# Kernel tuning notes

Measured on AMD Instinct MI355X. Metric: run time of the kernel, lower is better.

## Reference

```python
import jax, jax.numpy as jnp
import numpy as np

FEAT = 2048
NUM_CLASSES = 751
EPS = 1e-5


def setup_inputs() -> dict:
    key = jax.random.key(0)
    k1, k2, k3 = jax.random.split(key, 3)
    probe_x = jax.random.normal(k1, (64, FEAT), dtype=jnp.float32)
    gallery_x = jax.random.normal(k2, (256, FEAT), dtype=jnp.float32)
    # BatchNorm1d affine params (PyTorch init: gamma=1, beta=0)
    bn_gamma = jnp.ones((FEAT,), dtype=jnp.float32)
    bn_beta = jnp.zeros((FEAT,), dtype=jnp.float32)
    # classifier: weight ~ N(0, 0.001), bias = 0
    W = jax.random.normal(k3, (NUM_CLASSES, FEAT), dtype=jnp.float32) * 0.001
    b = jnp.zeros((NUM_CLASSES,), dtype=jnp.float32)
    return {"probe_x": probe_x, "gallery_x": gallery_x,
            "bn_gamma": bn_gamma, "bn_beta": bn_beta, "W": W, "b": b}


def reference(probe_x, gallery_x, bn_gamma, bn_beta, W, b):
    n_probe, feat = probe_x.shape
    n_gallery = gallery_x.shape[0]
    # broadcast squared difference: [Np, Ng, F]
    diff = jnp.square(probe_x[:, None, :] - gallery_x[None, :, :])
    d = diff.reshape(n_probe * n_gallery, feat)
    # BatchNorm1d in training mode: biased batch statistics over the batch dim
    mean = jnp.mean(d, axis=0)
    var = jnp.mean(jnp.square(d - mean), axis=0)
    bn = (d - mean) * (bn_gamma / jnp.sqrt(var + EPS)) + bn_beta
    # Linear classifier
    cls = jnp.einsum('nf,cf->nc', bn, W) + b
    return cls.reshape(n_probe, n_gallery, -1)
```

## Files before the change

kernel.cpp:

```cpp
#include <hip/hip_runtime.h>
#include <hip/hip_bf16.h>
#include <hip/hip_fp16.h>

#define FEAT 2048
#define NCLS 751
#define NPAD 768
#define NPRB 64
#define NGAL 256
#define WSCALE 256.0f

typedef _Float16 f16x8 __attribute__((ext_vector_type(8)));
typedef float f32x4 __attribute__((ext_vector_type(4)));

__device__ __forceinline__ unsigned short f2h_u(float x) {
  union { _Float16 h; unsigned short u; } v;
  v.h = (_Float16)x;
  return v.u;
}

__global__ __launch_bounds__(256)
void stats_kernel(const float* __restrict__ P, const float* __restrict__ G,
                  const float* __restrict__ gamma, const float* __restrict__ beta,
                  float* __restrict__ st) {
  const int t = threadIdx.x;
  const int fx = t & 7, ry = t >> 3;
  const int f = blockIdx.x * 8 + fx;
  float a1 = 0, a2 = 0, a3 = 0, a4 = 0;
#pragma unroll
  for (int r = ry; r < NPRB; r += 32) {
    float x = P[r * FEAT + f], x2 = x * x;
    a1 += x; a2 += x2; a3 += x2 * x; a4 += x2 * x2;
  }
  float b1 = 0, b2 = 0, b3 = 0, b4 = 0;
#pragma unroll
  for (int r = ry; r < NGAL; r += 32) {
    float x = G[r * FEAT + f], x2 = x * x;
    b1 += x; b2 += x2; b3 += x2 * x; b4 += x2 * x2;
  }
  __shared__ float red[8][32][8];
  __shared__ float red2[8][4][8];
  float vals[8] = {a1, a2, a3, a4, b1, b2, b3, b4};
#pragma unroll
  for (int m = 0; m < 8; ++m) red[m][ry][fx] = vals[m];
  __syncthreads();
  {
    int m = t >> 5, q = (t >> 3) & 3, fx2 = t & 7;
    float s = 0.f;
#pragma unroll
    for (int r = 0; r < 8; ++r) s += red[m][q * 8 + r][fx2];
    red2[m][q][fx2] = s;
  }
  __syncthreads();
  if (t < 8) {
    float mm[8];
#pragma unroll
    for (int m = 0; m < 8; ++m)
      mm[m] = red2[m][0][t] + red2[m][1][t] + red2[m][2][t] + red2[m][3][t];
    float M1p = mm[0] * (1.f / NPRB), M2p = mm[1] * (1.f / NPRB);
    float M3p = mm[2] * (1.f / NPRB), M4p = mm[3] * (1.f / NPRB);
    float M1g = mm[4] * (1.f / NGAL), M2g = mm[5] * (1.f / NGAL);
    float M3g = mm[6] * (1.f / NGAL), M4g = mm[7] * (1.f / NGAL);
    float mean = M2p - 2.f * M1p * M1g + M2g;
    float Ed2 = M4p - 4.f * M3p * M1g + 6.f * M2p * M2g - 4.f * M1p * M3g + M4g;
    float var = Ed2 - mean * mean;
    int ff = blockIdx.x * 8 + t;
    float sv = gamma[ff] / sqrtf(var + 1e-5f);
    st[ff] = sv;
    st[FEAT + ff] = beta[ff] - mean * sv;
  }
}

__global__ void prepw_kernel(const float* __restrict__ W, const float* __restrict__ b,
                             const float* __restrict__ st,
                             unsigned short* __restrict__ Wp, float* __restrict__ bp) {
  int c = blockIdx.x;
  int f = threadIdx.x * 8;
  float4 w0 = make_float4(0.f, 0.f, 0.f, 0.f), w1 = w0;
  if (c < NCLS) {
    const float4* wsrc = (const float4*)(W + (size_t)c * FEAT + f);
    w0 = wsrc[0]; w1 = wsrc[1];
  }
  const float4* s4 = (const float4*)(st + f);
  float4 s0 = s4[0], s1 = s4[1];
  const float4* t4 = (const float4*)(st + FEAT + f);
  float4 t0 = t4[0], t1 = t4[1];
  uint4 u;
  u.x = (unsigned int)f2h_u(w0.x * s0.x * WSCALE) | ((unsigned int)f2h_u(w0.y * s0.y * WSCALE) << 16);
  u.y = (unsigned int)f2h_u(w0.z * s0.z * WSCALE) | ((unsigned int)f2h_u(w0.w * s0.w * WSCALE) << 16);
  u.z = (unsigned int)f2h_u(w1.x * s1.x * WSCALE) | ((unsigned int)f2h_u(w1.y * s1.y * WSCALE) << 16);
  u.w = (unsigned int)f2h_u(w1.z * s1.z * WSCALE) | ((unsigned int)f2h_u(w1.w * s1.w * WSCALE) << 16);
  *(uint4*)(Wp + (size_t)c * FEAT + f) = u;
  float acc = t0.x * w0.x + t0.y * w0.y + t0.z * w0.z + t0.w * w0.w +
              t1.x * w1.x + t1.y * w1.y + t1.z * w1.z + t1.w * w1.w;
#pragma unroll
  for (int off = 32; off > 0; off >>= 1) acc += __shfl_down(acc, off, 64);
  __shared__ float r[4];
  int wave = threadIdx.x >> 6, lane = threadIdx.x & 63;
  if (lane == 0) r[wave] = acc;
  __syncthreads();
  if (threadIdx.x == 0) bp[c] = (c < NCLS ? b[c] : 0.f) + r[0] + r[1] + r[2] + r[3];
}

__global__ __launch_bounds__(512, 4)
void gemm_fused_kernel(const float* __restrict__ P, const float* __restrict__ G,
                       const unsigned short* __restrict__ Wp,
                       const float* __restrict__ bp, float* __restrict__ out) {
  __shared__ unsigned short As[2][128 * 32];
  __shared__ unsigned short Bs[2][192 * 32];

  const int tid = threadIdx.x;
  const int lane = tid & 63, wave = tid >> 6;
  const int mtile = blockIdx.x, ntile = blockIdx.y;
  const int p = mtile >> 1;

  const int arow = tid >> 2, ach = tid & 3;
  const int aoff = arow * 32 + ((ach ^ ((arow >> 1) & 3)) * 8);
  const float* gp = G + (size_t)((mtile & 1) * 128 + arow) * FEAT + ach * 8;
  const float* pp = P + (size_t)p * FEAT + ach * 8;

  const int bch = (lane & 3) ^ ((lane >> 3) & 3);
  const unsigned short* bg0 =
      Wp + (size_t)(ntile * 192 + wave * 16 + (lane >> 2)) * FEAT + bch * 8;
  const unsigned short* bg1 =
      Wp + (size_t)(ntile * 192 + 128 + wave * 16 + (lane >> 2)) * FEAT + bch * 8;
  const int bdo0 = wave * 1024;
  const int bdo1 = 8192 + wave * 1024;

  float4 ga, gb, pa, pb;
  ga = ((const float4*)gp)[0]; gb = ((const float4*)gp)[1];
  pa = ((const float4*)pp)[0]; pb = ((const float4*)pp)[1];
  __builtin_amdgcn_global_load_lds(
      (const __attribute__((address_space(1))) void*)bg0,
      (__attribute__((address_space(3))) void*)((char*)Bs[0] + bdo0), 16, 0, 0);
  if (wave < 4)
    __builtin_amdgcn_global_load_lds(
        (const __attribute__((address_space(1))) void*)bg1,
        (__attribute__((address_space(3))) void*)((char*)Bs[0] + bdo1), 16, 0, 0);
  {
    float d0 = pa.x - ga.x, d1 = pa.y - ga.y, d2 = pa.z - ga.z, d3 = pa.w - ga.w;
    float d4 = pb.x - gb.x, d5 = pb.y - gb.y, d6 = pb.z - gb.z, d7 = pb.w - gb.w;
    uint4 u;
    u.x = (unsigned int)f2h_u(d0 * d0) | ((unsigned int)f2h_u(d1 * d1) << 16);
    u.y = (unsigned int)f2h_u(d2 * d2) | ((unsigned int)f2h_u(d3 * d3) << 16);
    u.z = (unsigned int)f2h_u(d4 * d4) | ((unsigned int)f2h_u(d5 * d5) << 16);
    u.w = (unsigned int)f2h_u(d6 * d6) | ((unsigned int)f2h_u(d7 * d7) << 16);
    *(uint4*)(As[0] + aoff) = u;
  }
  __syncthreads();

  f32x4 acc[4][3];
#pragma unroll
  for (int mi = 0; mi < 4; ++mi)
#pragma unroll
    for (int ni = 0; ni < 3; ++ni) acc[mi][ni] = (f32x4){0.f, 0.f, 0.f, 0.f};

  const int wm = (wave & 1) * 64, wn = (wave >> 1) * 48;
  const int frow = lane & 15, fk = lane >> 4;
  const int fslot = fk ^ ((frow >> 1) & 3);

  int cur = 0;
  for (int t = 0; t < 64; ++t) {
    const int k0 = t * 32;
    const bool hn = (t < 63);

    if (hn) {
      const float* gn = gp + k0 + 32;
      const float* pn = pp + k0 + 32;
      ga = ((const float4*)gn)[0]; gb = ((const float4*)gn)[1];
      pa = ((const float4*)pn)[0]; pb = ((const float4*)pn)[1];
      __builtin_amdgcn_global_load_lds(
          (const __attribute__((address_space(1))) void*)(bg0 + k0 + 32),
          (__attribute__((address_space(3))) void*)((char*)Bs[cur ^ 1] + bdo0), 16, 0, 0);
      if (wave < 4)
        __builtin_amdgcn_global_load_lds(
            (const __attribute__((address_space(1))) void*)(bg1 + k0 + 32),
            (__attribute__((address_space(3))) void*)((char*)Bs[cur ^ 1] + bdo1), 16, 0, 0);
    }

    __builtin_amdgcn_s_setprio(1);
    {
      f16x8 af[4], bf[3];
#pragma unroll
      for (int mi = 0; mi < 4; ++mi)
        af[mi] = *(const f16x8*)(As[cur] + (wm + mi * 16 + frow) * 32 + fslot * 8);
#pragma unroll
      for (int ni = 0; ni < 3; ++ni)
        bf[ni] = *(const f16x8*)(Bs[cur] + (wn + ni * 16 + frow) * 32 + fslot * 8);
#pragma unroll
      for (int mi = 0; mi < 4; ++mi)
#pragma unroll
        for (int ni = 0; ni < 3; ++ni)
          acc[mi][ni] = __builtin_amdgcn_mfma_f32_16x16x32_f16(af[mi], bf[ni], acc[mi][ni], 0, 0, 0);
    }
    __builtin_amdgcn_s_setprio(0);

    if (hn) {
      float d0 = pa.x - ga.x, d1 = pa.y - ga.y, d2 = pa.z - ga.z, d3 = pa.w - ga.w;
      float d4 = pb.x - gb.x, d5 = pb.y - gb.y, d6 = pb.z - gb.z, d7 = pb.w - gb.w;
      uint4 u;
      u.x = (unsigned int)f2h_u(d0 * d0) | ((unsigned int)f2h_u(d1 * d1) << 16);
      u.y = (unsigned int)f2h_u(d2 * d2) | ((unsigned int)f2h_u(d3 * d3) << 16);
      u.z = (unsigned int)f2h_u(d4 * d4) | ((unsigned int)f2h_u(d5 * d5) << 16);
      u.w = (unsigned int)f2h_u(d6 * d6) | ((unsigned int)f2h_u(d7 * d7) << 16);
      *(uint4*)(As[cur ^ 1] + aoff) = u;
    }

    __syncthreads();
    cur ^= 1;
  }

  const int col0 = ntile * 192 + wn + (lane & 15);
  const int row0 = mtile * 128 + wm + ((lane >> 4) << 2);
#pragma unroll
  for (int ni = 0; ni < 3; ++ni) {
    int col = col0 + ni * 16;
    if (col >= NCLS) continue;
    float bv = bp[col];
#pragma unroll
    for (int mi = 0; mi < 4; ++mi) {
      int row = row0 + mi * 16;
#pragma unroll
      for (int r = 0; r < 4; ++r)
        out[(size_t)(row + r) * NCLS + col] = acc[mi][ni][r] * (1.0f / WSCALE) + bv;
    }
  }
}

extern "C" void kernel_launch(void* const* d_in, const int* in_sizes, int n_in,
                              void* d_out, int out_size, void* d_ws, size_t ws_size,
                              hipStream_t stream) {
  const float* P = (const float*)d_in[0];
  const float* G = (const float*)d_in[1];
  const float* gamma = (const float*)d_in[2];
  const float* beta = (const float*)d_in[3];
  const float* W = (const float*)d_in[4];
  const float* b = (const float*)d_in[5];
  float* out = (float*)d_out;

  float* st = (float*)d_ws;
  float* bp = st + 2 * FEAT;
  unsigned short* Wp = (unsigned short*)(bp + NPAD);

  hipLaunchKernelGGL(stats_kernel, dim3(256), dim3(256), 0, stream, P, G, gamma, beta, st);
  hipLaunchKernelGGL(prepw_kernel, dim3(NPAD), dim3(256), 0, stream, W, b, st, Wp, bp);
  hipLaunchKernelGGL(gemm_fused_kernel, dim3(128, 4), dim3(512), 0, stream, P, G, Wp, bp, out);
}
```

Baseline: 164.6 us.

## Keep A fragments in registers, triple-buffer W tiles, stage output through LDS

Each wave now computes its own 16-row A fragment (squared diff converted to fp16) straight into registers, so the A tile no longer goes through shared memory. Each wave covers all 192 columns instead of splitting the tile 2x4. W tiles are triple-buffered with async global-to-LDS loads two steps ahead, synchronised by manual vmcnt waits and raw barriers. The grid is remapped to 1D with a swizzle so blocks sharing W are spread across XCDs, and the epilogue stages results in LDS for row-contiguous stores. The risk is that every wave now reloads P and G from global memory redundantly, and the lower per-wave data reuse adds B-fragment LDS reads.

```diff
diff --git a/kernel.cpp b/kernel.cpp
--- a/kernel.cpp
+++ b/kernel.cpp
@@ -105,123 +105,138 @@
 void gemm_fused_kernel(const float* __restrict__ P, const float* __restrict__ G,
                        const unsigned short* __restrict__ Wp,
                        const float* __restrict__ bp, float* __restrict__ out) {
-  __shared__ unsigned short As[2][128 * 32];
-  __shared__ unsigned short Bs[2][192 * 32];
+  __shared__ unsigned short Bs[3][192 * 32];
 
   const int tid = threadIdx.x;
   const int lane = tid & 63, wave = tid >> 6;
-  const int mtile = blockIdx.x, ntile = blockIdx.y;
+  const int idp = (blockIdx.x & 7) * 64 + (blockIdx.x >> 3);
+  const int ntile = idp >> 7, mtile = idp & 127;
   const int p = mtile >> 1;
 
-  const int arow = tid >> 2, ach = tid & 3;
-  const int aoff = arow * 32 + ((ach ^ ((arow >> 1) & 3)) * 8);
-  const float* gp = G + (size_t)((mtile & 1) * 128 + arow) * FEAT + ach * 8;
-  const float* pp = P + (size_t)p * FEAT + ach * 8;
+  const int frow = lane & 15, fk = lane >> 4;
+  const int fslot = fk ^ ((frow >> 1) & 3);
+
+  const float* gptr = G + (size_t)((mtile & 1) * 128 + wave * 16 + frow) * FEAT + fk * 8;
+  const float* pptr = P + (size_t)p * FEAT + fk * 8;
 
   const int bch = (lane & 3) ^ ((lane >> 3) & 3);
-  const unsigned short* bg0 =
+  const unsigned short* wsrc =
       Wp + (size_t)(ntile * 192 + wave * 16 + (lane >> 2)) * FEAT + bch * 8;
-  const unsigned short* bg1 =
-      Wp + (size_t)(ntile * 192 + 128 + wave * 16 + (lane >> 2)) * FEAT + bch * 8;
-  const int bdo0 = wave * 1024;
-  const int bdo1 = 8192 + wave * 1024;
-
-  float4 ga, gb, pa, pb;
-  ga = ((const float4*)gp)[0]; gb = ((const float4*)gp)[1];
-  pa = ((const float4*)pp)[0]; pb = ((const float4*)pp)[1];
+  const unsigned short* wsrc2 = wsrc + (size_t)128 * FEAT;
+  const int bdo = wave * 1024;
+  const int bdo2 = 8192 + wave * 1024;
+
+  unsigned short* bsA = (unsigned short*)Bs[0];
+  unsigned short* bsB = (unsigned short*)Bs[1];
+  unsigned short* bsC = (unsigned short*)Bs[2];
+
   __builtin_amdgcn_global_load_lds(
-      (const __attribute__((address_space(1))) void*)bg0,
-      (__attribute__((address_space(3))) void*)((char*)Bs[0] + bdo0), 16, 0, 0);
+      (const __attribute__((address_space(1))) void*)wsrc,
+      (__attribute__((address_space(3))) void*)((char*)bsA + bdo), 16, 0, 0);
   if (wave < 4)
     __builtin_amdgcn_global_load_lds(
-        (const __attribute__((address_space(1))) void*)bg1,
-        (__attribute__((address_space(3))) void*)((char*)Bs[0] + bdo1), 16, 0, 0);
+        (const __attribute__((address_space(1))) void*)wsrc2,
+        (__attribute__((address_space(3))) void*)((char*)bsA + bdo2), 16, 0, 0);
+  float4 gA = ((const float4*)gptr)[0], gB = ((const float4*)gptr)[1];
+  float4 pA = ((const float4*)pptr)[0], pB = ((const float4*)pptr)[1];
+  __builtin_amdgcn_global_load_lds(
+      (const __attribute__((address_space(1))) void*)(wsrc + 32),
+      (__attribute__((address_space(3))) void*)((char*)bsB + bdo), 16, 0, 0);
+  if (wave < 4)
+    __builtin_amdgcn_global_load_lds(
+        (const __attribute__((address_space(1))) void*)(wsrc2 + 32),
+        (__attribute__((address_space(3))) void*)((char*)bsB + bdo2), 16, 0, 0);
+
+  f16x8 af;
   {
-    float d0 = pa.x - ga.x, d1 = pa.y - ga.y, d2 = pa.z - ga.z, d3 = pa.w - ga.w;
-    float d4 = pb.x - gb.x, d5 = pb.y - gb.y, d6 = pb.z - gb.z, d7 = pb.w - gb.w;
-    uint4 u;
-    u.x = (unsigned int)f2h_u(d0 * d0) | ((unsigned int)f2h_u(d1 * d1) << 16);
-    u.y = (unsigned int)f2h_u(d2 * d2) | ((unsigned int)f2h_u(d3 * d3) << 16);
-    u.z = (unsigned int)f2h_u(d4 * d4) | ((unsigned int)f2h_u(d5 * d5) << 16);
-    u.w = (unsigned int)f2h_u(d6 * d6) | ((unsigned int)f2h_u(d7 * d7) << 16);
-    *(uint4*)(As[0] + aoff) = u;
-  }
-  __syncthreads();
-
-  f32x4 acc[4][3];
-#pragma unroll
-  for (int mi = 0; mi < 4; ++mi)
-#pragma unroll
-    for (int ni = 0; ni < 3; ++ni) acc[mi][ni] = (f32x4){0.f, 0.f, 0.f, 0.f};
-
-  const int wm = (wave & 1) * 64, wn = (wave >> 1) * 48;
-  const int frow = lane & 15, fk = lane >> 4;
-  const int fslot = fk ^ ((frow >> 1) & 3);
-
-  int cur = 0;
+    float d0 = pA.x - gA.x, d1 = pA.y - gA.y, d2 = pA.z - gA.z, d3 = pA.w - gA.w;
+    float d4 = pB.x - gB.x, d5 = pB.y - gB.y, d6 = pB.z - gB.z, d7 = pB.w - gB.w;
+    af[0] = (_Float16)(d0 * d0); af[1] = (_Float16)(d1 * d1);
+    af[2] = (_Float16)(d2 * d2); af[3] = (_Float16)(d3 * d3);
+    af[4] = (_Float16)(d4 * d4); af[5] = (_Float16)(d5 * d5);
+    af[6] = (_Float16)(d6 * d6); af[7] = (_Float16)(d7 * d7);
+  }
+  asm volatile("s_waitcnt vmcnt(2)" ::: "memory");
+  __builtin_amdgcn_sched_barrier(0);
+  __builtin_amdgcn_s_barrier();
+  __builtin_amdgcn_sched_barrier(0);
+
+  f32x4 acc[12];
+#pragma unroll
+  for (int i = 0; i < 12; ++i) acc[i] = (f32x4){0.f, 0.f, 0.f, 0.f};
+
   for (int t = 0; t < 64; ++t) {
     const int k0 = t * 32;
-    const bool hn = (t < 63);
-
-    if (hn) {
-      const float* gn = gp + k0 + 32;
-      const float* pn = pp + k0 + 32;
-      ga = ((const float4*)gn)[0]; gb = ((const float4*)gn)[1];
-      pa = ((const float4*)pn)[0]; pb = ((const float4*)pn)[1];
+    if (t < 63) {
+      const float* gn = gptr + k0 + 32;
+      const float* pn = pptr + k0 + 32;
+      gA = ((const float4*)gn)[0]; gB = ((const float4*)gn)[1];
+      pA = ((const float4*)pn)[0]; pB = ((const float4*)pn)[1];
+    }
+    if (t < 62) {
       __builtin_amdgcn_global_load_lds(
-          (const __attribute__((address_space(1))) void*)(bg0 + k0 + 32),
-          (__attribute__((address_space(3))) void*)((char*)Bs[cur ^ 1] + bdo0), 16, 0, 0);
+          (const __attribute__((address_space(1))) void*)(wsrc + k0 + 64),
+          (__attribute__((address_space(3))) void*)((char*)bsC + bdo), 16, 0, 0);
       if (wave < 4)
         __builtin_amdgcn_global_load_lds(
-            (const __attribute__((address_space(1))) void*)(bg1 + k0 + 32),
-            (__attribute__((address_space(3))) void*)((char*)Bs[cur ^ 1] + bdo1), 16, 0, 0);
+            (const __attribute__((address_space(1))) void*)(wsrc2 + k0 + 64),
+            (__attribute__((address_space(3))) void*)((char*)bsC + bdo2), 16, 0, 0);
     }
 
     __builtin_amdgcn_s_setprio(1);
-    {
-      f16x8 af[4], bf[3];
-#pragma unroll
-      for (int mi = 0; mi < 4; ++mi)
-        af[mi] = *(const f16x8*)(As[cur] + (wm + mi * 16 + frow) * 32 + fslot * 8);
-#pragma unroll
-      for (int ni = 0; ni < 3; ++ni)
-        bf[ni] = *(const f16x8*)(Bs[cur] + (wn + ni * 16 + frow) * 32 + fslot * 8);
-#pragma unroll
-      for (int mi = 0; mi < 4; ++mi)
-#pragma unroll
-        for (int ni = 0; ni < 3; ++ni)
-          acc[mi][ni] = __builtin_amdgcn_mfma_f32_16x16x32_f16(af[mi], bf[ni], acc[mi][ni], 0, 0, 0);
+#pragma unroll
+    for (int c = 0; c < 3; ++c) {
+      f16x8 bf0 = *(const f16x8*)(bsA + ((c * 4 + 0) * 16 + frow) * 32 + fslot * 8);
+      f16x8 bf1 = *(const f16x8*)(bsA + ((c * 4 + 1) * 16 + frow) * 32 + fslot * 8);
+      f16x8 bf2 = *(const f16x8*)(bsA + ((c * 4 + 2) * 16 + frow) * 32 + fslot * 8);
+      f16x8 bf3 = *(const f16x8*)(bsA + ((c * 4 + 3) * 16 + frow) * 32 + fslot * 8);
+      acc[c * 4 + 0] = __builtin_amdgcn_mfma_f32_16x16x32_f16(af, bf0, acc[c * 4 + 0], 0, 0, 0);
+      acc[c * 4 + 1] = __builtin_amdgcn_mfma_f32_16x16x32_f16(af, bf1, acc[c * 4 + 1], 0, 0, 0);
+      acc[c * 4 + 2] = __builtin_amdgcn_mfma_f32_16x16x32_f16(af, bf2, acc[c * 4 + 2], 0, 0, 0);
+      acc[c * 4 + 3] = __builtin_amdgcn_mfma_f32_16x16x32_f16(af, bf3, acc[c * 4 + 3], 0, 0, 0);
     }
     __builtin_amdgcn_s_setprio(0);
 
-    if (hn) {
-      float d0 = pa.x - ga.x, d1 = pa.y - ga.y, d2 = pa.z - ga.z, d3 = pa.w - ga.w;
-      float d4 = pb.x - gb.x, d5 = pb.y - gb.y, d6 = pb.z - gb.z, d7 = pb.w - gb.w;
-      uint4 u;
-      u.x = (unsigned int)f2h_u(d0 * d0) | ((unsigned int)f2h_u(d1 * d1) << 16);
-      u.y = (unsigned int)f2h_u(d2 * d2) | ((unsigned int)f2h_u(d3 * d3) << 16);
-      u.z = (unsigned int)f2h_u(d4 * d4) | ((unsigned int)f2h_u(d5 * d5) << 16);
-      u.w = (unsigned int)f2h_u(d6 * d6) | ((unsigned int)f2h_u(d7 * d7) << 16);
-      *(uint4*)(As[cur ^ 1] + aoff) = u;
-    }
-
+    if (t < 63) {
+      float d0 = pA.x - gA.x, d1 = pA.y - gA.y, d2 = pA.z - gA.z, d3 = pA.w - gA.w;
+      float d4 = pB.x - gB.x, d5 = pB.y - gB.y, d6 = pB.z - gB.z, d7 = pB.w - gB.w;
+      af[0] = (_Float16)(d0 * d0); af[1] = (_Float16)(d1 * d1);
+      af[2] = (_Float16)(d2 * d2); af[3] = (_Float16)(d3 * d3);
+      af[4] = (_Float16)(d4 * d4); af[5] = (_Float16)(d5 * d5);
+      af[6] = (_Float16)(d6 * d6); af[7] = (_Float16)(d7 * d7);
+    }
+
+    asm volatile("s_waitcnt vmcnt(2)" ::: "memory");
+    __builtin_amdgcn_sched_barrier(0);
+    __builtin_amdgcn_s_barrier();
+    __builtin_amdgcn_sched_barrier(0);
+
+    unsigned short* tmp = bsA; bsA = bsB; bsB = bsC; bsC = tmp;
+  }
+
+  float* sf = (float*)Bs;
+  const int LW = 196;
+#pragma unroll 1
+  for (int c = 0; c < 4; ++c) {
     __syncthreads();
-    cur ^= 1;
-  }
-
-  const int col0 = ntile * 192 + wn + (lane & 15);
-  const int row0 = mtile * 128 + wm + ((lane >> 4) << 2);
-#pragma unroll
-  for (int ni = 0; ni < 3; ++ni) {
-    int col = col0 + ni * 16;
-    if (col >= NCLS) continue;
-    float bv = bp[col];
-#pragma unroll
-    for (int mi = 0; mi < 4; ++mi) {
-      int row = row0 + mi * 16;
-#pragma unroll
-      for (int r = 0; r < 4; ++r)
-        out[(size_t)(row + r) * NCLS + col] = acc[mi][ni][r] * (1.0f / WSCALE) + bv;
+    if ((wave >> 1) == c) {
+      const int lr0 = (wave & 1) * 16 + ((lane >> 4) << 2);
+      const int lc = lane & 15;
+#pragma unroll
+      for (int ni = 0; ni < 12; ++ni)
+#pragma unroll
+        for (int r = 0; r < 4; ++r)
+          sf[(lr0 + r) * LW + ni * 16 + lc] = acc[ni][r] * (1.0f / WSCALE);
+    }
+    __syncthreads();
+    const int grow0 = mtile * 128 + c * 32;
+#pragma unroll
+    for (int i = 0; i < 12; ++i) {
+      int u = tid + i * 512;
+      int row = u / 192, cin = u - row * 192;
+      int col = ntile * 192 + cin;
+      if (col < NCLS)
+        out[(size_t)(grow0 + row) * NCLS + col] = sf[row * LW + cin] + bp[col];
     }
   }
 }
@@ -243,5 +258,5 @@
 
   hipLaunchKernelGGL(stats_kernel, dim3(256), dim3(256), 0, stream, P, G, gamma, beta, st);
   hipLaunchKernelGGL(prepw_kernel, dim3(NPAD), dim3(256), 0, stream, W, b, st, Wp, bp);
-  hipLaunchKernelGGL(gemm_fused_kernel, dim3(128, 4), dim3(512), 0, stream, P, G, Wp, bp, out);
-}
+  hipLaunchKernelGGL(gemm_fused_kernel, dim3(512), dim3(512), 0, stream, P, G, Wp, bp, out);
+}
```

Measured after the change: 185.6 us. 12.8% more time.

## Stage GEMM epilogue through LDS for coalesced stores and remap blocks per XCD

Applied to the files above, without the earlier changes.

The output tile is now staged through shared memory in four 32-row chunks, so each row of 192 columns is written by consecutive threads. This replaces the scattered per-lane column stores of the MFMA layout with coalesced stores. The grid is flattened to 1D and remapped so blocks sharing an N tile land on the same XCD, which should improve L2 reuse of the packed weight tile. The price is extra barriers and LDS traffic in the epilogue, and the buffers are aliased into one raw shared array.

```diff
diff --git a/kernel.cpp b/kernel.cpp
--- a/kernel.cpp
+++ b/kernel.cpp
@@ -12,10 +12,10 @@
 typedef _Float16 f16x8 __attribute__((ext_vector_type(8)));
 typedef float f32x4 __attribute__((ext_vector_type(4)));
 
-__device__ __forceinline__ unsigned short f2h_u(float x) {
+__device__ __forceinline__ unsigned int f2h_u(float x) {
   union { _Float16 h; unsigned short u; } v;
   v.h = (_Float16)x;
-  return v.u;
+  return (unsigned int)v.u;
 }
 
 __global__ __launch_bounds__(256)
@@ -85,10 +85,10 @@
   const float4* t4 = (const float4*)(st + FEAT + f);
   float4 t0 = t4[0], t1 = t4[1];
   uint4 u;
-  u.x = (unsigned int)f2h_u(w0.x * s0.x * WSCALE) | ((unsigned int)f2h_u(w0.y * s0.y * WSCALE) << 16);
-  u.y = (unsigned int)f2h_u(w0.z * s0.z * WSCALE) | ((unsigned int)f2h_u(w0.w * s0.w * WSCALE) << 16);
-  u.z = (unsigned int)f2h_u(w1.x * s1.x * WSCALE) | ((unsigned int)f2h_u(w1.y * s1.y * WSCALE) << 16);
-  u.w = (unsigned int)f2h_u(w1.z * s1.z * WSCALE) | ((unsigned int)f2h_u(w1.w * s1.w * WSCALE) << 16);
+  u.x = f2h_u(w0.x * s0.x * WSCALE) | (f2h_u(w0.y * s0.y * WSCALE) << 16);
+  u.y = f2h_u(w0.z * s0.z * WSCALE) | (f2h_u(w0.w * s0.w * WSCALE) << 16);
+  u.z = f2h_u(w1.x * s1.x * WSCALE) | (f2h_u(w1.y * s1.y * WSCALE) << 16);
+  u.w = f2h_u(w1.z * s1.z * WSCALE) | (f2h_u(w1.w * s1.w * WSCALE) << 16);
   *(uint4*)(Wp + (size_t)c * FEAT + f) = u;
   float acc = t0.x * w0.x + t0.y * w0.y + t0.z * w0.z + t0.w * w0.w +
               t1.x * w1.x + t1.y * w1.y + t1.z * w1.z + t1.w * w1.w;
@@ -105,12 +105,18 @@
 void gemm_fused_kernel(const float* __restrict__ P, const float* __restrict__ G,
                        const unsigned short* __restrict__ Wp,
                        const float* __restrict__ bp, float* __restrict__ out) {
-  __shared__ unsigned short As[2][128 * 32];
-  __shared__ unsigned short Bs[2][192 * 32];
+  __shared__ __align__(16) char smem[40960];
+  unsigned short* As0 = (unsigned short*)smem;
+  unsigned short* As1 = (unsigned short*)(smem + 8192);
+  unsigned short* Bs0 = (unsigned short*)(smem + 16384);
+  unsigned short* Bs1 = (unsigned short*)(smem + 28672);
 
   const int tid = threadIdx.x;
   const int lane = tid & 63, wave = tid >> 6;
-  const int mtile = blockIdx.x, ntile = blockIdx.y;
+  const int bid = blockIdx.x;
+  const int xcd = bid & 7;
+  const int ntile = xcd >> 1;
+  const int mtile = (xcd & 1) * 64 + (bid >> 3);
   const int p = mtile >> 1;
 
   const int arow = tid >> 2, ach = tid & 3;
@@ -121,30 +127,28 @@
   const int bch = (lane & 3) ^ ((lane >> 3) & 3);
   const unsigned short* bg0 =
       Wp + (size_t)(ntile * 192 + wave * 16 + (lane >> 2)) * FEAT + bch * 8;
-  const unsigned short* bg1 =
-      Wp + (size_t)(ntile * 192 + 128 + wave * 16 + (lane >> 2)) * FEAT + bch * 8;
+  const unsigned short* bg1 = bg0 + (size_t)128 * FEAT;
   const int bdo0 = wave * 1024;
   const int bdo1 = 8192 + wave * 1024;
 
-  float4 ga, gb, pa, pb;
-  ga = ((const float4*)gp)[0]; gb = ((const float4*)gp)[1];
-  pa = ((const float4*)pp)[0]; pb = ((const float4*)pp)[1];
+  float4 ga = ((const float4*)gp)[0], gb = ((const float4*)gp)[1];
+  float4 pa = ((const float4*)pp)[0], pb = ((const float4*)pp)[1];
   __builtin_amdgcn_global_load_lds(
       (const __attribute__((address_space(1))) void*)bg0,
-      (__attribute__((address_space(3))) void*)((char*)Bs[0] + bdo0), 16, 0, 0);
+      (__attribute__((address_space(3))) void*)((char*)Bs0 + bdo0), 16, 0, 0);
   if (wave < 4)
     __builtin_amdgcn_global_load_lds(
         (const __attribute__((address_space(1))) void*)bg1,
-        (__attribute__((address_space(3))) void*)((char*)Bs[0] + bdo1), 16, 0, 0);
+        (__attribute__((address_space(3))) void*)((char*)Bs0 + bdo1), 16, 0, 0);
   {
     float d0 = pa.x - ga.x, d1 = pa.y - ga.y, d2 = pa.z - ga.z, d3 = pa.w - ga.w;
     float d4 = pb.x - gb.x, d5 = pb.y - gb.y, d6 = pb.z - gb.z, d7 = pb.w - gb.w;
     uint4 u;
-    u.x = (unsigned int)f2h_u(d0 * d0) | ((unsigned int)f2h_u(d1 * d1) << 16);
-    u.y = (unsigned int)f2h_u(d2 * d2) | ((unsigned int)f2h_u(d3 * d3) << 16);
-    u.z = (unsigned int)f2h_u(d4 * d4) | ((unsigned int)f2h_u(d5 * d5) << 16);
-    u.w = (unsigned int)f2h_u(d6 * d6) | ((unsigned int)f2h_u(d7 * d7) << 16);
-    *(uint4*)(As[0] + aoff) = u;
+    u.x = f2h_u(d0 * d0) | (f2h_u(d1 * d1) << 16);
+    u.y = f2h_u(d2 * d2) | (f2h_u(d3 * d3) << 16);
+    u.z = f2h_u(d4 * d4) | (f2h_u(d5 * d5) << 16);
+    u.w = f2h_u(d6 * d6) | (f2h_u(d7 * d7) << 16);
+    *(uint4*)(As0 + aoff) = u;
   }
   __syncthreads();
 
@@ -158,11 +162,10 @@
   const int frow = lane & 15, fk = lane >> 4;
   const int fslot = fk ^ ((frow >> 1) & 3);
 
-  int cur = 0;
+  unsigned short *Ac = As0, *An = As1, *Bc = Bs0, *Bn = Bs1;
   for (int t = 0; t < 64; ++t) {
     const int k0 = t * 32;
     const bool hn = (t < 63);
-
     if (hn) {
       const float* gn = gp + k0 + 32;
       const float* pn = pp + k0 + 32;
@@ -170,11 +173,11 @@
       pa = ((const float4*)pn)[0]; pb = ((const float4*)pn)[1];
       __builtin_amdgcn_global_load_lds(
           (const __attribute__((address_space(1))) void*)(bg0 + k0 + 32),
-          (__attribute__((address_space(3))) void*)((char*)Bs[cur ^ 1] + bdo0), 16, 0, 0);
+          (__attribute__((address_space(3))) void*)((char*)Bn + bdo0), 16, 0, 0);
       if (wave < 4)
         __builtin_amdgcn_global_load_lds(
             (const __attribute__((address_space(1))) void*)(bg1 + k0 + 32),
-            (__attribute__((address_space(3))) void*)((char*)Bs[cur ^ 1] + bdo1), 16, 0, 0);
+            (__attribute__((address_space(3))) void*)((char*)Bn + bdo1), 16, 0, 0);
     }
 
     __builtin_amdgcn_s_setprio(1);
@@ -182,10 +185,10 @@
       f16x8 af[4], bf[3];
 #pragma unroll
       for (int mi = 0; mi < 4; ++mi)
-        af[mi] = *(const f16x8*)(As[cur] + (wm + mi * 16 + frow) * 32 + fslot * 8);
+        af[mi] = *(const f16x8*)(Ac + (wm + mi * 16 + frow) * 32 + fslot * 8);
 #pragma unroll
       for (int ni = 0; ni < 3; ++ni)
-        bf[ni] = *(const f16x8*)(Bs[cur] + (wn + ni * 16 + frow) * 32 + fslot * 8);
+        bf[ni] = *(const f16x8*)(Bc + (wn + ni * 16 + frow) * 32 + fslot * 8);
 #pragma unroll
       for (int mi = 0; mi < 4; ++mi)
 #pragma unroll
@@ -198,30 +201,46 @@
       float d0 = pa.x - ga.x, d1 = pa.y - ga.y, d2 = pa.z - ga.z, d3 = pa.w - ga.w;
       float d4 = pb.x - gb.x, d5 = pb.y - gb.y, d6 = pb.z - gb.z, d7 = pb.w - gb.w;
       uint4 u;
-      u.x = (unsigned int)f2h_u(d0 * d0) | ((unsigned int)f2h_u(d1 * d1) << 16);
-      u.y = (unsigned int)f2h_u(d2 * d2) | ((unsigned int)f2h_u(d3 * d3) << 16);
-      u.z = (unsigned int)f2h_u(d4 * d4) | ((unsigned int)f2h_u(d5 * d5) << 16);
-      u.w = (unsigned int)f2h_u(d6 * d6) | ((unsigned int)f2h_u(d7 * d7) << 16);
-      *(uint4*)(As[cur ^ 1] + aoff) = u;
+      u.x = f2h_u(d0 * d0) | (f2h_u(d1 * d1) << 16);
+      u.y = f2h_u(d2 * d2) | (f2h_u(d3 * d3) << 16);
+      u.z = f2h_u(d4 * d4) | (f2h_u(d5 * d5) << 16);
+      u.w = f2h_u(d6 * d6) | (f2h_u(d7 * d7) << 16);
+      *(uint4*)(An + aoff) = u;
     }
 
     __syncthreads();
-    cur ^= 1;
-  }
-
-  const int col0 = ntile * 192 + wn + (lane & 15);
-  const int row0 = mtile * 128 + wm + ((lane >> 4) << 2);
-#pragma unroll
-  for (int ni = 0; ni < 3; ++ni) {
-    int col = col0 + ni * 16;
-    if (col >= NCLS) continue;
-    float bv = bp[col];
-#pragma unroll
-    for (int mi = 0; mi < 4; ++mi) {
-      int row = row0 + mi * 16;
-#pragma unroll
-      for (int r = 0; r < 4; ++r)
-        out[(size_t)(row + r) * NCLS + col] = acc[mi][ni][r] * (1.0f / WSCALE) + bv;
+    unsigned short* tm;
+    tm = Ac; Ac = An; An = tm;
+    tm = Bc; Bc = Bn; Bn = tm;
+  }
+
+  float* sf = (float*)smem;
+  const int LW = 196;
+  const int fq = lane >> 4, lc = lane & 15;
+#pragma unroll 1
+  for (int c = 0; c < 4; ++c) {
+    __syncthreads();
+    if ((wave & 1) == (c >> 1)) {
+#pragma unroll
+      for (int j = 0; j < 2; ++j) {
+        const int mi = (c & 1) * 2 + j;
+#pragma unroll
+        for (int ni = 0; ni < 3; ++ni)
+#pragma unroll
+          for (int r = 0; r < 4; ++r)
+            sf[(j * 16 + fq * 4 + r) * LW + wn + ni * 16 + lc] =
+                acc[mi][ni][r] * (1.0f / WSCALE);
+      }
+    }
+    __syncthreads();
+    const int grow0 = mtile * 128 + c * 32;
+#pragma unroll
+    for (int i = 0; i < 12; ++i) {
+      int u = tid + i * 512;
+      int row = u / 192, cin = u - row * 192;
+      int col = ntile * 192 + cin;
+      if (col < NCLS)
+        out[(size_t)(grow0 + row) * NCLS + col] = sf[row * LW + cin] + bp[col];
     }
   }
 }
@@ -243,5 +262,5 @@
 
   hipLaunchKernelGGL(stats_kernel, dim3(256), dim3(256), 0, stream, P, G, gamma, beta, st);
   hipLaunchKernelGGL(prepw_kernel, dim3(NPAD), dim3(256), 0, stream, W, b, st, Wp, bp);
-  hipLaunchKernelGGL(gemm_fused_kernel, dim3(128, 4), dim3(512), 0, stream, P, G, Wp, bp, out);
-}
+  hipLaunchKernelGGL(gemm_fused_kernel, dim3(512), dim3(512), 0, stream, P, G, Wp, bp, out);
+}
```

After: 534.7 us. +224.9%, slower.
